# Kernel optimization log

Measured on AMD Instinct MI355X. Metric: run time of the kernel, lower is better.

The kernel has to match this reference:

```python
import jax, jax.numpy as jnp
import numpy as np

IN_F, OUT_F = 512, 512
GRID_SIZE, SPLINE_ORDER = 5, 3
K = GRID_SIZE + SPLINE_ORDER  # 8 basis functions
B, S = 8, 1024


def setup_inputs() -> dict:
    key = jax.random.key(0)
    k1, k2, k3, k4, k5 = jax.random.split(key, 5)
    return {
        "x": jax.random.normal(k1, (B, S, IN_F), dtype=jnp.float32),
        "coeff": jax.random.normal(k2, (OUT_F, IN_F, K), dtype=jnp.float32),
        "scale_base": jax.random.normal(k3, (OUT_F, IN_F), dtype=jnp.float32) * 0.1,
        "scale_spline": jax.random.normal(k4, (OUT_F, IN_F), dtype=jnp.float32),
        "base_bias": jax.random.normal(k5, (OUT_F, IN_F), dtype=jnp.float32),
    }


def reference(x, coeff, scale_base, scale_spline, base_bias):
    batch = x.shape[0]
    in_f = x.shape[-1]
    k = coeff.shape[-1]

    xc = jnp.clip(x.reshape(-1, in_f), -1.0, 1.0)      # (N, in)
    base = jax.nn.silu(xc)                              # (N, in)

    # polynomial basis recurrence: b0 = 1, b1 = x, b_i = 2*x*b_{i-1} - 1
    bases = [jnp.ones_like(xc), xc]
    for _ in range(2, k):
        bases.append(2.0 * xc * bases[-1] - 1.0)
    basis = jnp.stack(bases[:k], axis=-1)               # (N, in, K)

    # spline[n,o] = sum_{i,k} scale_spline[o,i]*coeff[o,i,k]*basis[n,i,k]
    w_spline = scale_spline[..., None] * coeff          # (out, in, K)
    spline_term = jnp.einsum('nik,oik->no', basis, w_spline)
    base_term = base @ scale_base.T                     # (N, out)
    out = base_term + spline_term + jnp.sum(base_bias, axis=1)  # (N, out)

    out = out.reshape(batch, -1, base_bias.shape[0])    # (B, S, out)
    if out.shape[-2] == 1:
        out = out[..., 0, :]
    return out
```

## Files before the change

kernel.cpp:

```cpp
#include <hip/hip_runtime.h>
#include <hip/hip_bf16.h>

#define IN_FEAT 512
#define OUT_FEAT 512
#define NTOK 8192
#define KDIM 4096

typedef short bf16x8 __attribute__((ext_vector_type(8)));
typedef float f32x16 __attribute__((ext_vector_type(16)));

static __device__ inline short f2bf(float f) {
    union { float f; unsigned u; } v; v.f = f;
    unsigned u = v.u;
    u += 0x7fffu + ((u >> 16) & 1u);
    return (short)(u >> 16);
}

static __device__ inline unsigned pack2bf(float f0, float f1) {
    union { float f; unsigned u; } a, b; a.f = f0; b.f = f1;
    return __builtin_amdgcn_perm(b.u + 0x8000u, a.u + 0x8000u, 0x07060302u);
}

static __device__ inline bf16x8 gen_chunk(float xv) {
    float xc = fminf(fmaxf(xv, -1.f), 1.f);
    float e  = __expf(-xc);
    float bse = xc * __builtin_amdgcn_rcpf(1.f + e);
    float b2 = 2.f * xc * xc - 1.f;
    float b3 = 2.f * xc * b2 - 1.f;
    float b4 = 2.f * xc * b3 - 1.f;
    float b5 = 2.f * xc * b4 - 1.f;
    float b6 = 2.f * xc * b5 - 1.f;
    float b7 = 2.f * xc * b6 - 1.f;
    union { uint4 u; bf16x8 v; } r;
    r.u.x = pack2bf(bse, xc);
    r.u.y = pack2bf(b2, b3);
    r.u.z = pack2bf(b4, b5);
    r.u.w = pack2bf(b6, b7);
    return r.v;
}

static __device__ inline void gload_lds16(const short* g, short* l) {
    __builtin_amdgcn_global_load_lds(
        (const __attribute__((address_space(1))) unsigned int*)g,
        (__attribute__((address_space(3))) unsigned int*)l,
        16, 0, 0);
}

__global__ __launch_bounds__(256) void kan_prep(
    const float* __restrict__ coeff, const float* __restrict__ scale_base,
    const float* __restrict__ scale_spline, const float* __restrict__ base_bias,
    short* __restrict__ Wb, float* __restrict__ bias)
{
    int o = blockIdx.x;
    int tid = threadIdx.x;
    float local = 0.f;
#pragma unroll
    for (int rep = 0; rep < 2; ++rep) {
        int i = tid + rep * 256;
        size_t oi = (size_t)o * IN_FEAT + i;
        const float4* c4 = (const float4*)(coeff + oi * 8);
        float4 ca = c4[0], cb = c4[1];
        float ss = scale_spline[oi];
        float sb = scale_base[oi];
        local += base_bias[oi] + ss * ca.x;
        bf16x8 w;
        w[0] = f2bf(sb);
        w[1] = f2bf(ss * ca.y); w[2] = f2bf(ss * ca.z); w[3] = f2bf(ss * ca.w);
        w[4] = f2bf(ss * cb.x); w[5] = f2bf(ss * cb.y); w[6] = f2bf(ss * cb.z);
        w[7] = f2bf(ss * cb.w);
        *(bf16x8*)(Wb + (size_t)o * KDIM + (size_t)i * 8) = w;
    }
    __shared__ float red[4];
    for (int off = 32; off > 0; off >>= 1) local += __shfl_down(local, off, 64);
    int lane = tid & 63, wv = tid >> 6;
    if (lane == 0) red[wv] = local;
    __syncthreads();
    if (tid == 0) bias[o] = red[0] + red[1] + red[2] + red[3];
}

__global__ __launch_bounds__(256, 3) void kan_gemm14(
    const float* __restrict__ x, const short* __restrict__ Wb,
    const float* __restrict__ bias, float* __restrict__ out)
{
    __shared__ __align__(16) short POOL[20480];
    short* Bs = POOL;

    int tid = threadIdx.x;
    int nb = blockIdx.x & 7;
    int mb = blockIdx.x >> 3;
    int m0 = mb * 64, o0 = nb * 64;

    int lane = tid & 63, wv = tid >> 6;
    int kk = wv;
    int l31 = lane & 31, half = lane >> 5;
    int rm  = l31 & 15;

    f32x16 acc[2][2];
#pragma unroll
    for (int a = 0; a < 2; ++a)
#pragma unroll
        for (int b = 0; b < 2; ++b) acc[a][b] = (f32x16)0.f;

    int rl = lane >> 4, q = lane & 15;
    const short* pB0 = Wb + (size_t)(o0 + wv * 16 +  0 + rl) * KDIM + (size_t)(q ^ ( 0 + rl)) * 8;
    const short* pB1 = Wb + (size_t)(o0 + wv * 16 +  4 + rl) * KDIM + (size_t)(q ^ ( 4 + rl)) * 8;
    const short* pB2 = Wb + (size_t)(o0 + wv * 16 +  8 + rl) * KDIM + (size_t)(q ^ ( 8 + rl)) * 8;
    const short* pB3 = Wb + (size_t)(o0 + wv * 16 + 12 + rl) * KDIM + (size_t)(q ^ (12 + rl)) * 8;

    const float* xp0 = x + (size_t)(m0 + l31) * IN_FEAT + kk * 4;

    int s0 = kk * 4 + half, s1 = s0 + 2;
    int of00 = l31 * 128        + ((s0 ^ rm) * 8);
    int of01 = (32 + l31) * 128 + ((s0 ^ rm) * 8);
    int of10 = l31 * 128        + ((s1 ^ rm) * 8);
    int of11 = (32 + l31) * 128 + ((s1 ^ rm) * 8);

#define COMPUTE(CUR, P0, P1)                                                  \
    {                                                                         \
        const short* Bsc_ = Bs + (CUR) * 8192;                                \
        bf16x8 b00 = *(const bf16x8*)(Bsc_ + of00);                           \
        bf16x8 b01 = *(const bf16x8*)(Bsc_ + of01);                           \
        bf16x8 b10 = *(const bf16x8*)(Bsc_ + of10);                           \
        bf16x8 b11 = *(const bf16x8*)(Bsc_ + of11);                           \
        bf16x8 a00 = gen_chunk(half ? (P0).y : (P0).x);                       \
        bf16x8 a01 = gen_chunk(half ? (P1).y : (P1).x);                       \
        bf16x8 a10 = gen_chunk(half ? (P0).w : (P0).z);                       \
        bf16x8 a11 = gen_chunk(half ? (P1).w : (P1).z);                       \
        __builtin_amdgcn_s_setprio(1);                                        \
        acc[0][0] = __builtin_amdgcn_mfma_f32_32x32x16_bf16(a00, b00, acc[0][0], 0, 0, 0); \
        acc[0][1] = __builtin_amdgcn_mfma_f32_32x32x16_bf16(a00, b01, acc[0][1], 0, 0, 0); \
        acc[1][0] = __builtin_amdgcn_mfma_f32_32x32x16_bf16(a01, b00, acc[1][0], 0, 0, 0); \
        acc[1][1] = __builtin_amdgcn_mfma_f32_32x32x16_bf16(a01, b01, acc[1][1], 0, 0, 0); \
        acc[0][0] = __builtin_amdgcn_mfma_f32_32x32x16_bf16(a10, b10, acc[0][0], 0, 0, 0); \
        acc[0][1] = __builtin_amdgcn_mfma_f32_32x32x16_bf16(a10, b11, acc[0][1], 0, 0, 0); \
        acc[1][0] = __builtin_amdgcn_mfma_f32_32x32x16_bf16(a11, b10, acc[1][0], 0, 0, 0); \
        acc[1][1] = __builtin_amdgcn_mfma_f32_32x32x16_bf16(a11, b11, acc[1][1], 0, 0, 0); \
        __builtin_amdgcn_s_setprio(0);                                        \
    }

#define ITER(IT, CUR, PC0, PC1, PN0, PN1)                                     \
    {                                                                         \
        short* bd_ = Bs + ((CUR) ^ 1) * 8192 + wv * 2048;                     \
        const size_t bo_ = (size_t)((IT) + 1) * 128;                          \
        gload_lds16(pB0 + bo_, bd_);                                          \
        gload_lds16(pB1 + bo_, bd_ + 512);                                    \
        gload_lds16(pB2 + bo_, bd_ + 1024);                                   \
        gload_lds16(pB3 + bo_, bd_ + 1536);                                   \
        __builtin_amdgcn_sched_barrier(0);                                    \
        asm volatile("" ::: "memory");                                        \
        {                                                                     \
            const float* xq_ = xp0 + (size_t)((IT) + 1) * 16;                 \
            PN0 = *(const float4*)(xq_);                                      \
            PN1 = *(const float4*)(xq_ + 16384);                              \
        }                                                                     \
        __builtin_amdgcn_sched_barrier(0);                                    \
        asm volatile("s_waitcnt vmcnt(6)" ::: "memory");                      \
        __builtin_amdgcn_sched_barrier(0);                                    \
        COMPUTE(CUR, PC0, PC1);                                               \
        asm volatile("s_waitcnt vmcnt(2) lgkmcnt(0)" ::: "memory");           \
        __builtin_amdgcn_s_barrier();                                         \
        asm volatile("" ::: "memory");                                        \
    }

    float4 Pa0, Pa1, Pb0, Pb1;

    {
        short* bd_ = Bs + wv * 2048;
        gload_lds16(pB0, bd_);
        gload_lds16(pB1, bd_ + 512);
        gload_lds16(pB2, bd_ + 1024);
        gload_lds16(pB3, bd_ + 1536);
        __builtin_amdgcn_sched_barrier(0);
        asm volatile("" ::: "memory");
        Pa0 = *(const float4*)(xp0);
        Pa1 = *(const float4*)(xp0 + 16384);
        __builtin_amdgcn_sched_barrier(0);
        asm volatile("s_waitcnt vmcnt(2)" ::: "memory");
        __builtin_amdgcn_s_barrier();
        asm volatile("" ::: "memory");
    }

    for (int j = 0; j < 15; ++j) {
        ITER(2 * j,     0, Pa0, Pa1, Pb0, Pb1);
        ITER(2 * j + 1, 1, Pb0, Pb1, Pa0, Pa1);
    }
    ITER(30, 0, Pa0, Pa1, Pb0, Pb1);

    asm volatile("s_waitcnt vmcnt(0)" ::: "memory");
    __builtin_amdgcn_sched_barrier(0);
    COMPUTE(1, Pb0, Pb1);
#undef ITER
#undef COMPUTE

    float* rbuf = (float*)POOL;
    __syncthreads();
    if (kk >= 2) {
        float* s_ = rbuf + (size_t)(kk - 2) * 4224 + lane * 66;
#pragma unroll
        for (int fm = 0; fm < 2; ++fm)
#pragma unroll
            for (int fn = 0; fn < 2; ++fn)
#pragma unroll
                for (int r = 0; r < 16; ++r)
                    s_[(fm * 2 + fn) * 16 + r] = acc[fm][fn][r];
    }
    __syncthreads();
    if (kk < 2) {
        const float* s_ = rbuf + (size_t)kk * 4224 + lane * 66;
#pragma unroll
        for (int fm = 0; fm < 2; ++fm)
#pragma unroll
            for (int fn = 0; fn < 2; ++fn)
#pragma unroll
                for (int r = 0; r < 16; ++r)
                    acc[fm][fn][r] += s_[(fm * 2 + fn) * 16 + r];
    }
    __syncthreads();
    if (kk == 1) {
        float* s_ = rbuf + lane * 66;
#pragma unroll
        for (int fm = 0; fm < 2; ++fm)
#pragma unroll
            for (int fn = 0; fn < 2; ++fn)
#pragma unroll
                for (int r = 0; r < 16; ++r)
                    s_[(fm * 2 + fn) * 16 + r] = acc[fm][fn][r];
    }
    __syncthreads();
    if (kk == 0) {
        const float* s_ = rbuf + lane * 66;
#pragma unroll
        for (int fn = 0; fn < 2; ++fn) {
            int o = o0 + fn * 32 + l31;
            float bv = bias[o];
#pragma unroll
            for (int fm = 0; fm < 2; ++fm) {
#pragma unroll
                for (int r = 0; r < 16; ++r) {
                    float v = acc[fm][fn][r] + s_[(fm * 2 + fn) * 16 + r] + bv;
                    int token = m0 + fm * 32 + (r & 3) + 8 * (r >> 2) + 4 * half;
                    out[(size_t)token * OUT_FEAT + o] = v;
                }
            }
        }
    }
}

extern "C" void kernel_launch(void* const* d_in, const int* in_sizes, int n_in,
                              void* d_out, int out_size, void* d_ws, size_t ws_size,
                              hipStream_t stream) {
    const float* x            = (const float*)d_in[0];
    const float* coeff        = (const float*)d_in[1];
    const float* scale_base   = (const float*)d_in[2];
    const float* scale_spline = (const float*)d_in[3];
    const float* base_bias    = (const float*)d_in[4];
    float* out = (float*)d_out;

    short* Wb   = (short*)d_ws;
    float* bias = (float*)((char*)d_ws + (size_t)OUT_FEAT * KDIM * 2);

    kan_prep<<<OUT_FEAT, 256, 0, stream>>>(coeff, scale_base, scale_spline, base_bias, Wb, bias);
    kan_gemm14<<<(NTOK / 64) * (OUT_FEAT / 64), 256, 0, stream>>>(x, Wb, bias, out);
}
```

Baseline: 146.7 us.

## Triple-buffer B tiles in LDS with two-ahead prefetch and hardware bf16 pack

Changes the GEMM main loop from double to triple buffering. B tiles and x chunks are now prefetched two iterations ahead, and the per-iteration barrier is removed from between load issue and compute, so more global-load latency can hide behind MFMA work. Basis packing now uses the v_cvt_pk_bf16_f32 instruction in place of manual rounding plus a perm. LDS use grows to 48KB per block, which may limit occupancy, and the fewer waits make correctness depend on the vmcnt accounting.

Measured after the change: 135.9 us. -7.3%, faster.

```diff
diff --git a/kernel.cpp b/kernel.cpp
--- a/kernel.cpp
+++ b/kernel.cpp
@@ -16,9 +16,10 @@
     return (short)(u >> 16);
 }
 
-static __device__ inline unsigned pack2bf(float f0, float f1) {
-    union { float f; unsigned u; } a, b; a.f = f0; b.f = f1;
-    return __builtin_amdgcn_perm(b.u + 0x8000u, a.u + 0x8000u, 0x07060302u);
+static __device__ inline unsigned cvtpk(float lo, float hi) {
+    unsigned r;
+    asm("v_cvt_pk_bf16_f32 %0, %1, %2" : "=v"(r) : "v"(lo), "v"(hi));
+    return r;
 }
 
 static __device__ inline bf16x8 gen_chunk(float xv) {
@@ -32,10 +33,10 @@
     float b6 = 2.f * xc * b5 - 1.f;
     float b7 = 2.f * xc * b6 - 1.f;
     union { uint4 u; bf16x8 v; } r;
-    r.u.x = pack2bf(bse, xc);
-    r.u.y = pack2bf(b2, b3);
-    r.u.z = pack2bf(b4, b5);
-    r.u.w = pack2bf(b6, b7);
+    r.u.x = cvtpk(bse, xc);
+    r.u.y = cvtpk(b2, b3);
+    r.u.z = cvtpk(b4, b5);
+    r.u.w = cvtpk(b6, b7);
     return r.v;
 }
 
@@ -78,11 +79,11 @@
     if (tid == 0) bias[o] = red[0] + red[1] + red[2] + red[3];
 }
 
-__global__ __launch_bounds__(256, 3) void kan_gemm14(
+__global__ __launch_bounds__(256, 3) void kan_gemm15(
     const float* __restrict__ x, const short* __restrict__ Wb,
     const float* __restrict__ bias, float* __restrict__ out)
 {
-    __shared__ __align__(16) short POOL[20480];
+    __shared__ __align__(16) short POOL[24576];
     short* Bs = POOL;
 
     int tid = threadIdx.x;
@@ -138,58 +139,52 @@
         __builtin_amdgcn_s_setprio(0);                                        \
     }
 
-#define ITER(IT, CUR, PC0, PC1, PN0, PN1)                                     \
+#define ISSUE_B(DST, IT)                                                      \
     {                                                                         \
-        short* bd_ = Bs + ((CUR) ^ 1) * 8192 + wv * 2048;                     \
-        const size_t bo_ = (size_t)((IT) + 1) * 128;                          \
+        short* bd_ = Bs + (DST) * 8192 + wv * 2048;                           \
+        const size_t bo_ = (size_t)(IT) * 128;                                \
         gload_lds16(pB0 + bo_, bd_);                                          \
         gload_lds16(pB1 + bo_, bd_ + 512);                                    \
         gload_lds16(pB2 + bo_, bd_ + 1024);                                   \
         gload_lds16(pB3 + bo_, bd_ + 1536);                                   \
-        __builtin_amdgcn_sched_barrier(0);                                    \
-        asm volatile("" ::: "memory");                                        \
+    }
+
+#define ITER(IT, CUR, DST, PC0, PC1, PN0, PN1)                                \
+    {                                                                         \
+        ISSUE_B(DST, (IT) + 2);                                               \
         {                                                                     \
-            const float* xq_ = xp0 + (size_t)((IT) + 1) * 16;                 \
+            const float* xq_ = xp0 + (size_t)((IT) + 2) * 16;                 \
             PN0 = *(const float4*)(xq_);                                      \
             PN1 = *(const float4*)(xq_ + 16384);                              \
         }                                                                     \
-        __builtin_amdgcn_sched_barrier(0);                                    \
+        COMPUTE(CUR, PC0, PC1);                                               \
         asm volatile("s_waitcnt vmcnt(6)" ::: "memory");                      \
-        __builtin_amdgcn_sched_barrier(0);                                    \
-        COMPUTE(CUR, PC0, PC1);                                               \
-        asm volatile("s_waitcnt vmcnt(2) lgkmcnt(0)" ::: "memory");           \
         __builtin_amdgcn_s_barrier();                                         \
-        asm volatile("" ::: "memory");                                        \
-    }
-
-    float4 Pa0, Pa1, Pb0, Pb1;
-
-    {
-        short* bd_ = Bs + wv * 2048;
-        gload_lds16(pB0, bd_);
-        gload_lds16(pB1, bd_ + 512);
-        gload_lds16(pB2, bd_ + 1024);
-        gload_lds16(pB3, bd_ + 1536);
-        __builtin_amdgcn_sched_barrier(0);
-        asm volatile("" ::: "memory");
-        Pa0 = *(const float4*)(xp0);
-        Pa1 = *(const float4*)(xp0 + 16384);
-        __builtin_amdgcn_sched_barrier(0);
-        asm volatile("s_waitcnt vmcnt(2)" ::: "memory");
-        __builtin_amdgcn_s_barrier();
-        asm volatile("" ::: "memory");
-    }
-
-    for (int j = 0; j < 15; ++j) {
-        ITER(2 * j,     0, Pa0, Pa1, Pb0, Pb1);
-        ITER(2 * j + 1, 1, Pb0, Pb1, Pa0, Pa1);
-    }
-    ITER(30, 0, Pa0, Pa1, Pb0, Pb1);
-
+    }
+
+    float4 Pa0, Pa1, Pb0, Pb1, Pc0, Pc1;
+
+    ISSUE_B(0, 0);
+    Pa0 = *(const float4*)(xp0);
+    Pa1 = *(const float4*)(xp0 + 16384);
+    ISSUE_B(1, 1);
+    Pb0 = *(const float4*)(xp0 + 16);
+    Pb1 = *(const float4*)(xp0 + 16 + 16384);
+    asm volatile("s_waitcnt vmcnt(6)" ::: "memory");
+    __builtin_amdgcn_s_barrier();
+
+    for (int j = 0; j < 10; ++j) {
+        ITER(3 * j,     0, 2, Pa0, Pa1, Pc0, Pc1);
+        ITER(3 * j + 1, 1, 0, Pb0, Pb1, Pa0, Pa1);
+        ITER(3 * j + 2, 2, 1, Pc0, Pc1, Pb0, Pb1);
+    }
+
+    COMPUTE(0, Pa0, Pa1);
     asm volatile("s_waitcnt vmcnt(0)" ::: "memory");
-    __builtin_amdgcn_sched_barrier(0);
+    __builtin_amdgcn_s_barrier();
     COMPUTE(1, Pb0, Pb1);
 #undef ITER
+#undef ISSUE_B
 #undef COMPUTE
 
     float* rbuf = (float*)POOL;
@@ -260,5 +255,5 @@
     float* bias = (float*)((char*)d_ws + (size_t)OUT_FEAT * KDIM * 2);
 
     kan_prep<<<OUT_FEAT, 256, 0, stream>>>(coeff, scale_base, scale_spline, base_bias, Wb, bias);
-    kan_gemm14<<<(NTOK / 64) * (OUT_FEAT / 64), 256, 0, stream>>>(x, Wb, bias, out);
-}
+    kan_gemm15<<<(NTOK / 64) * (OUT_FEAT / 64), 256, 0, stream>>>(x, Wb, bias, out);
+}
```
